# Kernel tuning notes

Hardware: AMD Instinct MI355X
Metric: run time of the kernel (lower is better)

The kernel has to match this reference:

```python
import jax, jax.numpy as jnp
import numpy as np

N = 50000
E = 640000
R = 8


def setup_inputs() -> dict:
    key = jax.random.key(0)
    ks = jax.random.split(key, 12)
    in_c, hid_c, out_c = 128, 128, 64
    s1 = 1.0 / np.sqrt(in_c)
    s2 = 1.0 / np.sqrt(hid_c)
    s3 = 1.0 / np.sqrt(out_c)
    return {
        "x": jax.random.normal(ks[0], (N, in_c), dtype=jnp.float32),
        "edge_index": jax.random.randint(ks[1], (2, E), 0, N),
        "edge_type": jax.random.randint(ks[2], (E,), 0, R),
        # layer 1: per-relation weights, root weight, bias
        "W1": jax.random.uniform(ks[3], (R, in_c, hid_c), minval=-s1, maxval=s1, dtype=jnp.float32),
        "root1": jax.random.uniform(ks[4], (in_c, hid_c), minval=-s1, maxval=s1, dtype=jnp.float32),
        "b1": jnp.zeros((hid_c,), dtype=jnp.float32),
        # layer 2
        "W2": jax.random.uniform(ks[5], (R, hid_c, out_c), minval=-s2, maxval=s2, dtype=jnp.float32),
        "root2": jax.random.uniform(ks[6], (hid_c, out_c), minval=-s2, maxval=s2, dtype=jnp.float32),
        "b2": jnp.zeros((out_c,), dtype=jnp.float32),
        # classifier
        "Wc": jax.random.uniform(ks[7], (out_c, 2), minval=-s3, maxval=s3, dtype=jnp.float32),
        "bc": jnp.zeros((2,), dtype=jnp.float32),
    }


def _rgcn_layer(x, edge_index, edge_type, W, root, b):
    # PyG RGCNConv with aggr='mean': per relation r, mean-aggregate source
    # features over edges of type r into destinations, then apply W_r.
    # out = sum_r mean_agg_r(x) @ W_r + x @ root + b
    src, dst = edge_index[0], edge_index[1]
    msgs = x[src]  # [E, Fin] gather
    seg = edge_type * N + dst  # combined (relation, dst) segment id
    sums = jax.ops.segment_sum(msgs, seg, num_segments=R * N)  # [R*N, Fin]
    cnt = jax.ops.segment_sum(jnp.ones((msgs.shape[0],), x.dtype), seg, num_segments=R * N)
    mean = sums / jnp.maximum(cnt, 1.0)[:, None]  # zero-degree -> 0
    mean = mean.reshape(R, N, x.shape[1])  # [R, N, Fin]
    out = jnp.einsum("rnf,rfo->no", mean, W) + x @ root + b
    return out


def reference(x, edge_index, edge_type, W1, root1, b1, W2, root2, b2, Wc, bc):
    h = jax.nn.relu(_rgcn_layer(x, edge_index, edge_type, W1, root1, b1))
    # dropout (p=0.3) is identity in eval mode
    h = jax.nn.relu(_rgcn_layer(h, edge_index, edge_type, W2, root2, b2))
    logits = h @ Wc + bc  # [N, 2]
    return logits
```

## Files before the change

kernel.cpp:

```cpp
#include <hip/hip_runtime.h>

#define NN 50000
#define EE 640000
#define RR 8
#define CAP 64

typedef __bf16 bf16x8 __attribute__((ext_vector_type(8)));
typedef float  f32x4  __attribute__((ext_vector_type(4)));
typedef const __attribute__((address_space(1))) unsigned int* gas_p;
typedef __attribute__((address_space(3))) unsigned int* las_p;

__device__ __forceinline__ unsigned short f2b(float f) {
  unsigned int u = __float_as_uint(f);
  u += 0x7fffu + ((u >> 16) & 1u);
  return (unsigned short)(u >> 16);
}
__device__ __forceinline__ float b2f(unsigned short h) {
  return __uint_as_float(((unsigned int)h) << 16);
}

__device__ __forceinline__ float edge_scale(unsigned int e, int lane, int deg) {
  unsigned long long valid = __ballot(lane < deg);
  unsigned long long m0 = __ballot((e >> 16) & 1u);
  unsigned long long m1 = __ballot((e >> 17) & 1u);
  unsigned long long m2 = __ballot((e >> 18) & 1u);
  unsigned long long mm = ((e >> 16) & 1u ? m0 : ~m0);
  mm &= ((e >> 17) & 1u ? m1 : ~m1);
  mm &= ((e >> 18) & 1u ? m2 : ~m2);
  mm &= valid;
  return (lane < deg) ? __builtin_amdgcn_rcpf((float)__popcll(mm)) : 0.f;
}

#define CONV_N 1600000
#define B1_N (1152 * 128)
#define B2_N (640 * 128)
__global__ void k_prologue(const float* __restrict__ x, unsigned short* __restrict__ xb,
                           const float* __restrict__ W1, const float* __restrict__ root1,
                           unsigned short* __restrict__ B1T,
                           const float* __restrict__ W2, const float* __restrict__ root2,
                           unsigned short* __restrict__ B2T) {
  int t = blockIdx.x * 256 + threadIdx.x;
  if (t < CONV_N) {
    float4 v = reinterpret_cast<const float4*>(x)[t];
    ushort4 o = make_ushort4(f2b(v.x), f2b(v.y), f2b(v.z), f2b(v.w));
    reinterpret_cast<ushort4*>(xb)[t] = o;
    return;
  }
  t -= CONV_N;
  if (t < B1_N) {
    int j = t >> 7, k = t & 127;
    float v = (j < 1024) ? W1[((j >> 7) << 14) + (k << 7) + (j & 127)]
                         : root1[(k << 7) + (j - 1024)];
    B1T[t] = f2b(v);
    return;
  }
  t -= B1_N;
  if (t < B2_N) {
    int j = t >> 7, k = t & 127;
    float v = 0.0f;
    if (j < 512)      v = W2[((j >> 6) << 13) + (k << 6) + (j & 63)];
    else if (j < 576) v = root2[(k << 6) + (j - 512)];
    B2T[t] = f2b(v);
  }
}

#define NBG1 1173
#define NBE  2500
#define FSPLIT (3 * NBG1)

template <bool EDGES>
__global__ __launch_bounds__(256, 3) void k_gemm(
    const unsigned short* __restrict__ A, const unsigned short* __restrict__ BT,
    unsigned short* __restrict__ Y, float* __restrict__ rootOut,
    const float* __restrict__ bias, int M, int nsplit, int nroot, int nsub,
    const int* __restrict__ srcI, const int* __restrict__ dstI,
    const int* __restrict__ typ, int* __restrict__ cursor,
    unsigned int* __restrict__ entries) {
  __shared__ __align__(16) unsigned short Bs[2][64 * 128];
  const int tid = threadIdx.x;

  int bg;
  if (EDGES) {
    const int bid = blockIdx.x;
    int be = -1;
    if (bid < FSPLIT) {
      if (bid % 3 == 0) bg = bid / 3;
      else              be = 2 * (bid / 3) + (bid % 3) - 1;
    } else {
      be = 2 * NBG1 + (bid - FSPLIT);
    }
    if (be >= 0) {
      int e = be * 256 + tid;
      if (e < EE) {
        int d = dstI[e], r = typ[e];
        int pos = atomicAdd(&cursor[d], 1);
        if (pos < CAP)
          entries[d * CAP + pos] = (unsigned int)srcI[e] | ((unsigned int)r << 16);
      }
      return;
    }
  } else {
    bg = blockIdx.x;
  }

  const int m0 = (bg % 391) * 128;
  const int n0g = (bg / 391) * nsub * 64;
  const int lane = tid & 63;
  const int wave = tid >> 6;
  const int wm = (wave >> 1) << 6;
  const int wn = (wave & 1) << 5;
  const int l15 = lane & 15;
  const int quad = lane >> 4;

  {
    const unsigned short* Gb = BT + (size_t)n0g * 128;
#pragma unroll
    for (int c = 0; c < 4; ++c) {
      int L = tid + c * 256;
      int r = L >> 4, c16 = L & 15;
      int j = c16 ^ (r & 15);
      __builtin_amdgcn_global_load_lds(
          (gas_p)(const void*)(Gb + (size_t)r * 128 + j * 8),
          (las_p)(void*)(Bs[0] + r * 128 + c16 * 8), 16, 0, 0);
    }
  }

  bf16x8 af[4][4];
#pragma unroll
  for (int kk = 0; kk < 4; ++kk)
#pragma unroll
    for (int i = 0; i < 4; ++i)
      af[kk][i] = *reinterpret_cast<const bf16x8*>(
          A + (size_t)(m0 + wm + i * 16 + l15) * 128 + (kk * 4 + quad) * 8);

  __syncthreads();

  const int tr = lane >> 2;
  const int tc = lane & 3;
  const int sl0 = ((tc & 1) << 1) * 16 + tr;
  const int sl1 = sl0 + 16;
  const bool thi = (tc & 2) != 0;

  int buf = 0;
  for (int s = 0; s < nsub; ++s) {
    if (s + 1 < nsub) {
      const unsigned short* Gb = BT + (size_t)(n0g + (s + 1) * 64) * 128;
      unsigned short* Lb = Bs[buf ^ 1];
#pragma unroll
      for (int c = 0; c < 4; ++c) {
        int L = tid + c * 256;
        int r = L >> 4, c16 = L & 15;
        int j = c16 ^ (r & 15);
        __builtin_amdgcn_global_load_lds(
            (gas_p)(const void*)(Gb + (size_t)r * 128 + j * 8),
            (las_p)(void*)(Lb + r * 128 + c16 * 8), 16, 0, 0);
      }
    }

    f32x4 acc[4][2] = {};
    const unsigned short* Bc = Bs[buf];
#pragma unroll
    for (int kk = 0; kk < 4; ++kk) {
      const int sw = ((kk * 4 + quad) ^ l15) * 8;
      bf16x8 bfr[2];
#pragma unroll
      for (int j = 0; j < 2; ++j)
        bfr[j] = *reinterpret_cast<const bf16x8*>(&Bc[(wn + j * 16 + l15) * 128 + sw]);
#pragma unroll
      for (int i = 0; i < 4; ++i)
#pragma unroll
        for (int j = 0; j < 2; ++j)
          acc[i][j] = __builtin_amdgcn_mfma_f32_16x16x32_bf16(bfr[j], af[kk][i], acc[i][j], 0, 0, 0);
    }
    __syncthreads();

    const int scol = n0g + s * 64;
    if (scol >= nsplit) {
#pragma unroll
      for (int i = 0; i < 4; ++i) {
        const int m = wm + i * 16 + l15;
        if (m0 + m >= M) continue;
#pragma unroll
        for (int j = 0; j < 2; ++j) {
          const int col = scol + wn + j * 16 + quad * 4 - nsplit;
          if (col < nroot) {
            float4 b4 = *reinterpret_cast<const float4*>(&bias[col]);
            float4 v = make_float4(acc[i][j][0] + b4.x, acc[i][j][1] + b4.y,
                                   acc[i][j][2] + b4.z, acc[i][j][3] + b4.w);
            *reinterpret_cast<float4*>(&rootOut[(size_t)(m0 + m) * nroot + col]) = v;
          }
        }
      }
    } else {
#pragma unroll
      for (int i = 0; i < 4; ++i) {
        uint2 pk0, pk1;
        pk0.x = (unsigned int)f2b(acc[i][0][0]) | ((unsigned int)f2b(acc[i][0][1]) << 16);
        pk0.y = (unsigned int)f2b(acc[i][0][2]) | ((unsigned int)f2b(acc[i][0][3]) << 16);
        pk1.x = (unsigned int)f2b(acc[i][1][0]) | ((unsigned int)f2b(acc[i][1][1]) << 16);
        pk1.y = (unsigned int)f2b(acc[i][1][2]) | ((unsigned int)f2b(acc[i][1][3]) << 16);
        unsigned int a0x = __shfl(pk0.x, sl0, 64), a0y = __shfl(pk0.y, sl0, 64);
        unsigned int a1x = __shfl(pk1.x, sl0, 64), a1y = __shfl(pk1.y, sl0, 64);
        unsigned int b0x = __shfl(pk0.x, sl1, 64), b0y = __shfl(pk0.y, sl1, 64);
        unsigned int b1x = __shfl(pk1.x, sl1, 64), b1y = __shfl(pk1.y, sl1, 64);
        uint4 o;
        o.x = thi ? a1x : a0x;
        o.y = thi ? a1y : a0y;
        o.z = thi ? b1x : b0x;
        o.w = thi ? b1y : b0y;
        const int m = wm + i * 16 + tr;
        if (m0 + m < M)
          *reinterpret_cast<uint4*>(&Y[(size_t)(m0 + m) * nsplit + scol + wn + tc * 8]) = o;
      }
    }
    buf ^= 1;
  }
}

#define ACC8(pk, s)                                          \
  a[0] += b2f((unsigned short)pk.x) * s;                     \
  a[1] += __uint_as_float(pk.x & 0xffff0000u) * s;           \
  a[2] += b2f((unsigned short)pk.y) * s;                     \
  a[3] += __uint_as_float(pk.y & 0xffff0000u) * s;           \
  a[4] += b2f((unsigned short)pk.z) * s;                     \
  a[5] += __uint_as_float(pk.z & 0xffff0000u) * s;           \
  a[6] += b2f((unsigned short)pk.w) * s;                     \
  a[7] += __uint_as_float(pk.w & 0xffff0000u) * s;

__global__ void k_agg1(const unsigned int* __restrict__ entries,
                       const int* __restrict__ cursor,
                       const unsigned short* __restrict__ y,
                       const float* __restrict__ hpre,
                       unsigned int* __restrict__ hbf) {
  const int d = blockIdx.x * 4 + (threadIdx.x >> 6);
  const int lane = threadIdx.x & 63;
  int deg = cursor[d];
  if (deg > CAP) deg = CAP;
  unsigned int e = (lane < deg) ? entries[d * CAP + lane] : 0u;
  float sc = edge_scale(e, lane, deg);

  const int g = lane >> 4;
  const int l16 = lane & 15;

  float4 h0, h1;
  if (g == 0) {
    const float4* hp = reinterpret_cast<const float4*>(hpre) + (size_t)d * 32 + l16 * 2;
    h0 = hp[0];
    h1 = hp[1];
  }

  float a[8] = {};
  const int T = (deg + 15) >> 4;
  for (int t = 0; t < T; ++t) {
    const int base = t * 16 + g;
    unsigned int e0 = __shfl(e, base, 64);       float s0 = __shfl(sc, base, 64);
    unsigned int e1 = __shfl(e, base + 4, 64);   float s1 = __shfl(sc, base + 4, 64);
    unsigned int e2 = __shfl(e, base + 8, 64);   float s2 = __shfl(sc, base + 8, 64);
    unsigned int e3 = __shfl(e, base + 12, 64);  float s3 = __shfl(sc, base + 12, 64);
    uint4 p0 = *reinterpret_cast<const uint4*>(
        y + (((size_t)(e0 & 0xffffu)) << 10) + (((e0 >> 16) & 7u) << 7) + (l16 << 3));
    uint4 p1 = *reinterpret_cast<const uint4*>(
        y + (((size_t)(e1 & 0xffffu)) << 10) + (((e1 >> 16) & 7u) << 7) + (l16 << 3));
    uint4 p2 = *reinterpret_cast<const uint4*>(
        y + (((size_t)(e2 & 0xffffu)) << 10) + (((e2 >> 16) & 7u) << 7) + (l16 << 3));
    uint4 p3 = *reinterpret_cast<const uint4*>(
        y + (((size_t)(e3 & 0xffffu)) << 10) + (((e3 >> 16) & 7u) << 7) + (l16 << 3));
    ACC8(p0, s0);
    ACC8(p1, s1);
    ACC8(p2, s2);
    ACC8(p3, s3);
  }
#pragma unroll
  for (int j = 0; j < 8; ++j) {
    a[j] += __shfl_xor(a[j], 16, 64);
    a[j] += __shfl_xor(a[j], 32, 64);
  }
  if (g == 0) {
    float v0 = fmaxf(a[0] + h0.x, 0.f), v1 = fmaxf(a[1] + h0.y, 0.f);
    float v2 = fmaxf(a[2] + h0.z, 0.f), v3 = fmaxf(a[3] + h0.w, 0.f);
    float v4 = fmaxf(a[4] + h1.x, 0.f), v5 = fmaxf(a[5] + h1.y, 0.f);
    float v6 = fmaxf(a[6] + h1.z, 0.f), v7 = fmaxf(a[7] + h1.w, 0.f);
    uint4 o;
    o.x = (unsigned int)f2b(v0) | ((unsigned int)f2b(v1) << 16);
    o.y = (unsigned int)f2b(v2) | ((unsigned int)f2b(v3) << 16);
    o.z = (unsigned int)f2b(v4) | ((unsigned int)f2b(v5) << 16);
    o.w = (unsigned int)f2b(v6) | ((unsigned int)f2b(v7) << 16);
    reinterpret_cast<uint4*>(hbf)[(size_t)d * 16 + l16] = o;
  }
}

__global__ void k_agg2(const unsigned int* __restrict__ entries,
                       const int* __restrict__ cursor,
                       const unsigned short* __restrict__ y,
                       const float* __restrict__ hpre,
                       const float* __restrict__ Wc, const float* __restrict__ bc,
                       float* __restrict__ out) {
  const int d = blockIdx.x * 4 + (threadIdx.x >> 6);
  const int lane = threadIdx.x & 63;
  int deg = cursor[d];
  if (deg > CAP) deg = CAP;
  unsigned int e = (lane < deg) ? entries[d * CAP + lane] : 0u;
  float sc = edge_scale(e, lane, deg);

  const int g = lane >> 3;
  const int l8 = lane & 7;

  const float4* hp = reinterpret_cast<const float4*>(hpre) + (size_t)d * 16 + l8 * 2;
  float4 h0 = hp[0];
  float4 h1 = hp[1];

  float a[8] = {};
  const int T = (deg + 31) >> 5;
  for (int t = 0; t < T; ++t) {
    const int base = t * 32 + g;
    unsigned int e0 = __shfl(e, base, 64);       float s0 = __shfl(sc, base, 64);
    unsigned int e1 = __shfl(e, base + 8, 64);   float s1 = __shfl(sc, base + 8, 64);
    unsigned int e2 = __shfl(e, base + 16, 64);  float s2 = __shfl(sc, base + 16, 64);
    unsigned int e3 = __shfl(e, base + 24, 64);  float s3 = __shfl(sc, base + 24, 64);
    uint4 p0 = *reinterpret_cast<const uint4*>(
        y + (((size_t)(e0 & 0xffffu)) << 9) + (((e0 >> 16) & 7u) << 6) + (l8 << 3));
    uint4 p1 = *reinterpret_cast<const uint4*>(
        y + (((size_t)(e1 & 0xffffu)) << 9) + (((e1 >> 16) & 7u) << 6) + (l8 << 3));
    uint4 p2 = *reinterpret_cast<const uint4*>(
        y + (((size_t)(e2 & 0xffffu)) << 9) + (((e2 >> 16) & 7u) << 6) + (l8 << 3));
    uint4 p3 = *reinterpret_cast<const uint4*>(
        y + (((size_t)(e3 & 0xffffu)) << 9) + (((e3 >> 16) & 7u) << 6) + (l8 << 3));
    ACC8(p0, s0);
    ACC8(p1, s1);
    ACC8(p2, s2);
    ACC8(p3, s3);
  }
#pragma unroll
  for (int j = 0; j < 8; ++j) {
    a[j] += __shfl_xor(a[j], 8, 64);
    a[j] += __shfl_xor(a[j], 16, 64);
    a[j] += __shfl_xor(a[j], 32, 64);
  }
  float v0 = fmaxf(a[0] + h0.x, 0.f), v1 = fmaxf(a[1] + h0.y, 0.f);
  float v2 = fmaxf(a[2] + h0.z, 0.f), v3 = fmaxf(a[3] + h0.w, 0.f);
  float v4 = fmaxf(a[4] + h1.x, 0.f), v5 = fmaxf(a[5] + h1.y, 0.f);
  float v6 = fmaxf(a[6] + h1.z, 0.f), v7 = fmaxf(a[7] + h1.w, 0.f);
  const float4* wc4 = reinterpret_cast<const float4*>(Wc) + l8 * 4;
  float4 w0 = wc4[0], w1 = wc4[1], w2 = wc4[2], w3 = wc4[3];
  float p0 = v0 * w0.x + v1 * w0.z + v2 * w1.x + v3 * w1.z
           + v4 * w2.x + v5 * w2.z + v6 * w3.x + v7 * w3.z;
  float p1 = v0 * w0.y + v1 * w0.w + v2 * w1.y + v3 * w1.w
           + v4 * w2.y + v5 * w2.w + v6 * w3.y + v7 * w3.w;
  p0 += __shfl_xor(p0, 1, 64); p1 += __shfl_xor(p1, 1, 64);
  p0 += __shfl_xor(p0, 2, 64); p1 += __shfl_xor(p1, 2, 64);
  p0 += __shfl_xor(p0, 4, 64); p1 += __shfl_xor(p1, 4, 64);
  if (lane == 0) {
    out[d * 2 + 0] = p0 + bc[0];
    out[d * 2 + 1] = p1 + bc[1];
  }
}

extern "C" void kernel_launch(void* const* d_in, const int* in_sizes, int n_in,
                              void* d_out, int out_size, void* d_ws, size_t ws_size,
                              hipStream_t stream) {
  const float* x     = (const float*)d_in[0];
  const int*   ei    = (const int*)d_in[1];
  const int*   et    = (const int*)d_in[2];
  const float* W1    = (const float*)d_in[3];
  const float* root1 = (const float*)d_in[4];
  const float* b1    = (const float*)d_in[5];
  const float* W2    = (const float*)d_in[6];
  const float* root2 = (const float*)d_in[7];
  const float* b2    = (const float*)d_in[8];
  const float* Wc    = (const float*)d_in[9];
  const float* bc    = (const float*)d_in[10];
  const int* srcI = ei;
  const int* dstI = ei + EE;

  char* ws = (char*)d_ws;
  unsigned short* xb      = (unsigned short*)(ws);
  unsigned int*   hbf     = (unsigned int*)(ws);
  unsigned short* B1T     = (unsigned short*)(ws + 12800000);
  unsigned short* B2T     = (unsigned short*)(ws + 13094912);
  int*            cursor  = (int*)(ws + 13258752);
  unsigned int*   entries = (unsigned int*)(ws + 13458752);
  float*          hpre    = (float*)(ws + 26258752);
  unsigned short* y1      = (unsigned short*)(ws + 51858752);
  unsigned short* y2      = y1;

  hipMemsetAsync(cursor, 0, 200000, stream);

  const int PRO_N = CONV_N + B1_N + B2_N;
  k_prologue<<<(PRO_N + 255) / 256, 256, 0, stream>>>(x, xb, W1, root1, B1T,
                                                      W2, root2, B2T);

  k_gemm<true><<<dim3(NBG1 + NBE), 256, 0, stream>>>(xb, B1T, y1, hpre, b1,
                                                     NN, 1024, 128, 6,
                                                     srcI, dstI, et, cursor, entries);
  k_agg1<<<NN / 4, 256, 0, stream>>>(entries, cursor, y1, hpre, hbf);

  k_gemm<false><<<dim3(391 * 2), 256, 0, stream>>>((const unsigned short*)hbf, B2T, y2, hpre, b2,
                                                   NN, 512, 64, 5,
                                                   nullptr, nullptr, nullptr, nullptr, nullptr);
  k_agg2<<<NN / 4, 256, 0, stream>>>(entries, cursor, y2, hpre, Wc, bc, (float*)d_out);
}
```

Before: 247.0 us.

## Fuse x bf16 conversion into layer-1 GEMM A loads and fold cursor memset

The separate prologue pass that converted x from fp32 to bf16 into a workspace buffer is removed. The layer-1 GEMM now reads fp32 rows of x directly and rounds them to bf16 in registers, which saves writing and re-reading a bf16 copy of x. The cursor zeroing moves from a hipMemsetAsync into the prologue kernel, removing one launch. Both GEMMs also clamp A row indices to M-1 so loads past the last row stay in bounds. In exchange, the GEMM's A fetch reads twice as many bytes and does the conversion work inline.

```diff
diff --git a/kernel.cpp b/kernel.cpp
--- a/kernel.cpp
+++ b/kernel.cpp
@@ -31,22 +31,14 @@
   return (lane < deg) ? __builtin_amdgcn_rcpf((float)__popcll(mm)) : 0.f;
 }
 
-#define CONV_N 1600000
 #define B1_N (1152 * 128)
 #define B2_N (640 * 128)
-__global__ void k_prologue(const float* __restrict__ x, unsigned short* __restrict__ xb,
-                           const float* __restrict__ W1, const float* __restrict__ root1,
+__global__ void k_prologue(const float* __restrict__ W1, const float* __restrict__ root1,
                            unsigned short* __restrict__ B1T,
                            const float* __restrict__ W2, const float* __restrict__ root2,
-                           unsigned short* __restrict__ B2T) {
+                           unsigned short* __restrict__ B2T,
+                           int* __restrict__ cursor) {
   int t = blockIdx.x * 256 + threadIdx.x;
-  if (t < CONV_N) {
-    float4 v = reinterpret_cast<const float4*>(x)[t];
-    ushort4 o = make_ushort4(f2b(v.x), f2b(v.y), f2b(v.z), f2b(v.w));
-    reinterpret_cast<ushort4*>(xb)[t] = o;
-    return;
-  }
-  t -= CONV_N;
   if (t < B1_N) {
     int j = t >> 7, k = t & 127;
     float v = (j < 1024) ? W1[((j >> 7) << 14) + (k << 7) + (j & 127)]
@@ -61,16 +53,19 @@
     if (j < 512)      v = W2[((j >> 6) << 13) + (k << 6) + (j & 63)];
     else if (j < 576) v = root2[(k << 6) + (j - 512)];
     B2T[t] = f2b(v);
-  }
+    return;
+  }
+  t -= B2_N;
+  if (t < NN) cursor[t] = 0;
 }
 
 #define NBG1 1173
 #define NBE  2500
 #define FSPLIT (3 * NBG1)
 
-template <bool EDGES>
+template <bool EDGES, bool AF32>
 __global__ __launch_bounds__(256, 3) void k_gemm(
-    const unsigned short* __restrict__ A, const unsigned short* __restrict__ BT,
+    const void* __restrict__ A, const unsigned short* __restrict__ BT,
     unsigned short* __restrict__ Y, float* __restrict__ rootOut,
     const float* __restrict__ bias, int M, int nsplit, int nroot, int nsub,
     const int* __restrict__ srcI, const int* __restrict__ dstI,
@@ -126,12 +121,36 @@
   }
 
   bf16x8 af[4][4];
-#pragma unroll
-  for (int kk = 0; kk < 4; ++kk)
-#pragma unroll
-    for (int i = 0; i < 4; ++i)
-      af[kk][i] = *reinterpret_cast<const bf16x8*>(
-          A + (size_t)(m0 + wm + i * 16 + l15) * 128 + (kk * 4 + quad) * 8);
+  if (AF32) {
+    const float* Af = (const float*)A;
+#pragma unroll
+    for (int kk = 0; kk < 4; ++kk)
+#pragma unroll
+      for (int i = 0; i < 4; ++i) {
+        int rA = m0 + wm + i * 16 + l15;
+        if (rA > M - 1) rA = M - 1;
+        const float* p = Af + (size_t)rA * 128 + (kk * 4 + quad) * 8;
+        float4 q0 = *reinterpret_cast<const float4*>(p);
+        float4 q1 = *reinterpret_cast<const float4*>(p + 4);
+        uint4 u;
+        u.x = (unsigned int)f2b(q0.x) | ((unsigned int)f2b(q0.y) << 16);
+        u.y = (unsigned int)f2b(q0.z) | ((unsigned int)f2b(q0.w) << 16);
+        u.z = (unsigned int)f2b(q1.x) | ((unsigned int)f2b(q1.y) << 16);
+        u.w = (unsigned int)f2b(q1.z) | ((unsigned int)f2b(q1.w) << 16);
+        af[kk][i] = *reinterpret_cast<bf16x8*>(&u);
+      }
+  } else {
+    const unsigned short* Ab = (const unsigned short*)A;
+#pragma unroll
+    for (int kk = 0; kk < 4; ++kk)
+#pragma unroll
+      for (int i = 0; i < 4; ++i) {
+        int rA = m0 + wm + i * 16 + l15;
+        if (rA > M - 1) rA = M - 1;
+        af[kk][i] = *reinterpret_cast<const bf16x8*>(
+            Ab + (size_t)rA * 128 + (kk * 4 + quad) * 8);
+      }
+  }
 
   __syncthreads();
 
@@ -373,7 +392,6 @@
   const int* dstI = ei + EE;
 
   char* ws = (char*)d_ws;
-  unsigned short* xb      = (unsigned short*)(ws);
   unsigned int*   hbf     = (unsigned int*)(ws);
   unsigned short* B1T     = (unsigned short*)(ws + 12800000);
   unsigned short* B2T     = (unsigned short*)(ws + 13094912);
@@ -383,19 +401,17 @@
   unsigned short* y1      = (unsigned short*)(ws + 51858752);
   unsigned short* y2      = y1;
 
-  hipMemsetAsync(cursor, 0, 200000, stream);
-
-  const int PRO_N = CONV_N + B1_N + B2_N;
-  k_prologue<<<(PRO_N + 255) / 256, 256, 0, stream>>>(x, xb, W1, root1, B1T,
-                                                      W2, root2, B2T);
-
-  k_gemm<true><<<dim3(NBG1 + NBE), 256, 0, stream>>>(xb, B1T, y1, hpre, b1,
-                                                     NN, 1024, 128, 6,
-                                                     srcI, dstI, et, cursor, entries);
+  const int PRO_N = B1_N + B2_N + NN;
+  k_prologue<<<(PRO_N + 255) / 256, 256, 0, stream>>>(W1, root1, B1T,
+                                                      W2, root2, B2T, cursor);
+
+  k_gemm<true, true><<<dim3(NBG1 + NBE), 256, 0, stream>>>(
+      (const void*)x, B1T, y1, hpre, b1, NN, 1024, 128, 6,
+      srcI, dstI, et, cursor, entries);
   k_agg1<<<NN / 4, 256, 0, stream>>>(entries, cursor, y1, hpre, hbf);
 
-  k_gemm<false><<<dim3(391 * 2), 256, 0, stream>>>((const unsigned short*)hbf, B2T, y2, hpre, b2,
-                                                   NN, 512, 64, 5,
-                                                   nullptr, nullptr, nullptr, nullptr, nullptr);
+  k_gemm<false, false><<<dim3(391 * 2), 256, 0, stream>>>(
+      (const void*)hbf, B2T, y2, hpre, b2, NN, 512, 64, 5,
+      nullptr, nullptr, nullptr, nullptr, nullptr);
   k_agg2<<<NN / 4, 256, 0, stream>>>(entries, cursor, y2, hpre, Wc, bc, (float*)d_out);
 }
```

After: 262.3 us. 6.2% more time.
